# Performance work log

Measured on AMD Instinct MI355X. Metric: run time of the kernel, lower is better.

Reference implementation:

```python
import jax, jax.numpy as jnp
import numpy as np

B, T, C = 8, 2048, 1024  # micro_bsz, seq_len, n_embd (== complexsize)


def setup_inputs() -> dict:
    key = jax.random.key(0)
    ks = jax.random.split(key, 6)
    w = lambda k, shape: (jax.random.normal(k, shape, dtype=jnp.float32) * 0.02)
    return {
        "x": jax.random.normal(ks[0], (B, T, C), dtype=jnp.float32),
        "Wk": w(ks[1], (2 * C, C)),      # key: n_embd -> 2*n_embd (no bias)
        "Wa": w(ks[2], (C, 2 * C)),      # activation: 2*n_embd -> n_embd (no bias)
        "Wf": w(ks[3], (2, C, C)),       # WaveNet filter conv, kernel=2, WIO layout
        "Wg": w(ks[4], (2, C, C)),       # WaveNet gate conv, kernel=2, WIO layout
        "Wo": w(ks[5], (C, C)),          # WaveNet 1x1 output projection
    }


def _causal_conv(x, W):
    # x: [B,T,Cin], W: [K,Cin,Cout]; left-pad K-1 for causality
    return jax.lax.conv_general_dilated(
        x, W, window_strides=(1,), padding=[(W.shape[0] - 1, 0)],
        dimension_numbers=("NWC", "WIO", "NWC"))


def _wavenet_short(x, Wf, Wg, Wo):
    # undialated gated WaveNet unit: tanh(conv_f(x)) * sigmoid(conv_g(x)) -> 1x1 proj
    h = jnp.tanh(_causal_conv(x, Wf)) * jax.nn.sigmoid(_causal_conv(x, Wg))
    return h @ Wo.T


def reference(x, Wk, Wa, Wf, Wg, Wo):
    Bx, Tx, Cx = x.shape
    k = (x @ Wk.T).reshape(Bx, Tx, Cx, 2)                 # [B,T,C,2]
    cv = jax.lax.complex(k[..., 0], k[..., 1])            # view_as_complex -> [B,T,C]
    scale = jax.lax.cummax(jnp.abs(cv), axis=1)           # running max of magnitude
    cv2 = cv / scale.astype(cv.dtype)                      # normalize magnitude <= 1
    kv = jnp.cumprod(cv2, axis=1)                          # complex cumulative product
    re = jnp.stack([kv.real, kv.imag], axis=-1).reshape(Bx, Tx, 2 * Cx)  # view_as_real
    return (re @ Wa.T) * _wavenet_short(x * scale, Wf, Wg, Wo)
```

## Files before the change

### kernel.cpp

```cpp
#include <hip/hip_runtime.h>
#include <cmath>

#define T_SEQ 2048
#define C_DIM 1024

typedef unsigned short u16;
typedef unsigned int u32;
typedef short bf16x8 __attribute__((ext_vector_type(8)));
typedef _Float16 f16x8 __attribute__((ext_vector_type(8)));
typedef float f32x4 __attribute__((ext_vector_type(4)));
typedef unsigned short u16x8 __attribute__((ext_vector_type(8)));

#define AS1 __attribute__((address_space(1)))
#define AS3 __attribute__((address_space(3)))

__device__ __forceinline__ u16 f2bf(float f) {
    u32 u = __builtin_bit_cast(u32, f);
    u32 r = u + 0x7fffu + ((u >> 16) & 1u);
    return (u16)(r >> 16);
}
__device__ __forceinline__ u16 f2h(float f) {
    return __builtin_bit_cast(u16, (_Float16)f);
}
__device__ __forceinline__ float h2f(u16 h) {
    return (float)__builtin_bit_cast(_Float16, h);
}
__device__ __forceinline__ void gl_lds16(const void* g, void* l) {
    __builtin_amdgcn_global_load_lds((const AS1 u32*)g, (AS3 u32*)l, 16, 0, 0);
}

__device__ __forceinline__ int xcd_swz(int lin, int nwg) {
    return (lin & 7) * (nwg >> 3) + (lin >> 3);
}

#define SBAR() do { __builtin_amdgcn_sched_barrier(0); \
                    __builtin_amdgcn_s_barrier(); \
                    __builtin_amdgcn_sched_barrier(0); } while (0)
#define VMC(n) do { asm volatile("s_waitcnt vmcnt(" #n ")" ::: "memory"); \
                    __builtin_amdgcn_sched_barrier(0); } while (0)
#define LGKM0() do { asm volatile("s_waitcnt lgkmcnt(0)" ::: "memory"); \
                     __builtin_amdgcn_sched_barrier(0); } while (0)

template<int DT, int EPI>
__global__ __launch_bounds__(512, 2)
void gemm8(const u16* __restrict__ Ap, const u16* __restrict__ Bp,
           void* __restrict__ Cout, const u16* __restrict__ Cmul,
           int M, int N, int K)
{
    __shared__ u16 lds[2 * 32768];
    const int tid  = threadIdx.x;
    const int lane = tid & 63;
    const int wid  = tid >> 6;
    const int wrow = wid >> 2;
    const int wcol = wid & 3;
    const int gx = gridDim.x;
    const int lin = xcd_swz(blockIdx.x + gx * blockIdx.y, gx * gridDim.y);
    const int m0 = (lin / gx) * 256;
    const int n0 = (lin % gx) * 256;
    const int NT = K / 64;

    f32x4 acc[8][4] = {};

    auto stageu = [&](int t, int u) {
        const int isB = u & 1, kh = u >> 1;
        u16* ubase = &lds[(t & 1) * 32768 + isB * 16384 + kh * 8192];
        const u16* src = isB ? Bp + (size_t)n0 * K : Ap + (size_t)m0 * K;
        const int k0 = t * 64 + kh * 32;
        #pragma unroll
        for (int j = 0; j < 2; ++j) {
            const int c = wid + 8 * j;
            const int p = c * 64 + lane;
            const int row = p >> 2;
            const int sp  = (p & 3) ^ ((row >> 1) & 3);
            gl_lds16(src + (size_t)row * K + k0 + sp * 8, ubase + c * 512);
        }
    };

    auto lda = [&](int buf, int kh, int mq, u16x8 (&a)[4]) {
        const u16* base = &lds[buf * 32768 + kh * 8192];
        #pragma unroll
        for (int f = 0; f < 4; ++f) {
            const int row = wrow * 128 + mq * 64 + f * 16 + (lane & 15);
            const int sp  = (lane >> 4) ^ ((row >> 1) & 3);
            a[f] = *(const u16x8*)&base[row * 32 + sp * 8];
        }
    };
    auto ldb = [&](int buf, int kh, u16x8 (&b)[4]) {
        const u16* base = &lds[buf * 32768 + 16384 + kh * 8192];
        #pragma unroll
        for (int f = 0; f < 4; ++f) {
            const int row = wcol * 64 + f * 16 + (lane & 15);
            const int sp  = (lane >> 4) ^ ((row >> 1) & 3);
            b[f] = *(const u16x8*)&base[row * 32 + sp * 8];
        }
    };
    auto mm = [&](const u16x8 (&a)[4], const u16x8 (&b)[4], int mq) {
        __builtin_amdgcn_s_setprio(1);
        #pragma unroll
        for (int fm = 0; fm < 4; ++fm)
            #pragma unroll
            for (int fn = 0; fn < 4; ++fn) {
                if constexpr (DT == 1)
                    acc[mq * 4 + fm][fn] = __builtin_amdgcn_mfma_f32_16x16x32_f16(
                        __builtin_bit_cast(f16x8, a[fm]), __builtin_bit_cast(f16x8, b[fn]),
                        acc[mq * 4 + fm][fn], 0, 0, 0);
                else
                    acc[mq * 4 + fm][fn] = __builtin_amdgcn_mfma_f32_16x16x32_bf16(
                        __builtin_bit_cast(bf16x8, a[fm]), __builtin_bit_cast(bf16x8, b[fn]),
                        acc[mq * 4 + fm][fn], 0, 0, 0);
            }
        __builtin_amdgcn_s_setprio(0);
    };

    stageu(0, 0); stageu(0, 1); stageu(0, 2); stageu(0, 3);
    VMC(0);
    SBAR();

    u16x8 a[4], b[4];
    for (int t = 0; t < NT; ++t) {
        const int buf = t & 1;
        const bool more = (t + 1 < NT);
        lda(buf, 0, 0, a); ldb(buf, 0, b);
        if (more) stageu(t + 1, 0);
        SBAR(); LGKM0();
        mm(a, b, 0);
        SBAR();
        lda(buf, 0, 1, a);
        if (more) { stageu(t + 1, 1); VMC(4); } else { VMC(0); }
        SBAR(); LGKM0();
        mm(a, b, 1);
        SBAR();
        lda(buf, 1, 0, a); ldb(buf, 1, b);
        if (more) stageu(t + 1, 2);
        SBAR(); LGKM0();
        mm(a, b, 0);
        SBAR();
        lda(buf, 1, 1, a);
        if (more) { stageu(t + 1, 3); VMC(4); }
        SBAR(); LGKM0();
        mm(a, b, 1);
        SBAR();
    }

    const int crow0 = m0 + wrow * 128 + ((lane >> 4) << 2);
    const int ccol  = n0 + wcol * 64 + (lane & 15);
    #pragma unroll
    for (int mi = 0; mi < 8; ++mi)
        #pragma unroll
        for (int fn = 0; fn < 4; ++fn)
            #pragma unroll
            for (int r = 0; r < 4; ++r) {
                const size_t idx = (size_t)(crow0 + mi * 16 + r) * N + ccol + fn * 16;
                if constexpr (EPI == 0)
                    ((u16*)Cout)[idx] = f2h(acc[mi][fn][r]);
                else
                    ((float*)Cout)[idx] = h2f(Cmul[idx]) * acc[mi][fn][r];
            }
}

__global__ __launch_bounds__(512, 2)
void conv8(const u16* __restrict__ A, const u16* __restrict__ Wfgt,
           u16* __restrict__ H, int M)
{
    __shared__ u16 lds[2 * 32768];
    const int tid  = threadIdx.x;
    const int lane = tid & 63;
    const int wid  = tid >> 6;
    const int wrow = wid >> 1;
    const int wcol = wid & 1;
    const int gx = gridDim.x;
    const int lin = xcd_swz(blockIdx.x + gx * blockIdx.y, gx * gridDim.y);
    const int m0 = (lin / gx) * 256;
    const int n0 = (lin % gx) * 128;
    const int NT = 32;

    f32x4 accF[4][4] = {};
    f32x4 accG[4][4] = {};

    auto stageA = [&](int t, int kh) {
        u16* ubase = &lds[(t & 1) * 32768 + kh * 8192];
        const int tap = t >> 4;
        const int k0 = (t & 15) * 64 + kh * 32;
        const int sh = (tap == 0) ? 1 : 0;
        #pragma unroll
        for (int j = 0; j < 2; ++j) {
            const int c = wid + 8 * j;
            const int p = c * 64 + lane;
            const int row = p >> 2;
            const int sp  = (p & 3) ^ ((row >> 1) & 3);
            int grow = m0 + row - sh;
            if (grow < 0) grow = 0;
            gl_lds16(A + (size_t)grow * C_DIM + k0 + sp * 8, ubase + c * 512);
        }
    };
    auto stageB = [&](int t, int kh) {
        u16* ubase = &lds[(t & 1) * 32768 + 16384 + kh * 8192];
        const int tap = t >> 4;
        const int k0 = (t & 15) * 64 + kh * 32;
        const u16* BF = Wfgt + (size_t)tap * 2 * C_DIM * C_DIM;
        const u16* BG = BF + (size_t)C_DIM * C_DIM;
        #pragma unroll
        for (int j = 0; j < 2; ++j) {
            const int c = wid + 8 * j;
            const int isG = c >> 3;
            const int p = (c & 7) * 64 + lane;
            const int row = p >> 2;
            const int sp  = (p & 3) ^ ((row >> 1) & 3);
            const u16* src = (isG ? BG : BF) + (size_t)(n0 + row) * C_DIM + k0 + sp * 8;
            gl_lds16(src, ubase + isG * 4096 + (c & 7) * 512);
        }
    };

    auto lda4 = [&](int buf, int kh, bf16x8 (&a)[4]) {
        const u16* base = &lds[buf * 32768 + kh * 8192];
        #pragma unroll
        for (int f = 0; f < 4; ++f) {
            const int row = wrow * 64 + f * 16 + (lane & 15);
            const int sp  = (lane >> 4) ^ ((row >> 1) & 3);
            a[f] = *(const bf16x8*)&base[row * 32 + sp * 8];
        }
    };
    auto ldb4 = [&](int buf, int kh, int isG, bf16x8 (&b)[4]) {
        const u16* base = &lds[buf * 32768 + 16384 + kh * 8192 + isG * 4096];
        #pragma unroll
        for (int f = 0; f < 4; ++f) {
            const int row = wcol * 64 + f * 16 + (lane & 15);
            const int sp  = (lane >> 4) ^ ((row >> 1) & 3);
            b[f] = *(const bf16x8*)&base[row * 32 + sp * 8];
        }
    };
    auto mm4 = [&](const bf16x8 (&a)[4], const bf16x8 (&b)[4], f32x4 (&acc)[4][4]) {
        #pragma unroll
        for (int fm = 0; fm < 4; ++fm)
            #pragma unroll
            for (int fn = 0; fn < 4; ++fn)
                acc[fm][fn] = __builtin_amdgcn_mfma_f32_16x16x32_bf16(
                    a[fm], b[fn], acc[fm][fn], 0, 0, 0);
    };

    const bool zrow = (m0 % T_SEQ) == 0;
    const bool zlane = (wrow == 0) && ((lane & 15) == 0);
    const bf16x8 zvec = {0,0,0,0,0,0,0,0};

    stageA(0, 0); stageB(0, 0); stageA(0, 1); stageB(0, 1);
    VMC(0);
    SBAR();

    bf16x8 a[4], bF[4], bG[4];
    for (int t = 0; t < NT; ++t) {
        const int buf = t & 1;
        const bool more = (t + 1 < NT);
        const bool z0 = zrow && (t < 16);
        lda4(buf, 0, a); ldb4(buf, 0, 0, bF); ldb4(buf, 0, 1, bG);
        if (more) { stageA(t + 1, 0); stageB(t + 1, 0); VMC(4); } else { VMC(0); }
        SBAR(); LGKM0();
        if (z0 && zlane) a[0] = zvec;
        __builtin_amdgcn_s_setprio(1);
        mm4(a, bF, accF); mm4(a, bG, accG);
        __builtin_amdgcn_s_setprio(0);
        SBAR();
        lda4(buf, 1, a); ldb4(buf, 1, 0, bF); ldb4(buf, 1, 1, bG);
        if (more) { stageA(t + 1, 1); stageB(t + 1, 1); VMC(4); } else { VMC(0); }
        SBAR(); LGKM0();
        if (z0 && zlane) a[0] = zvec;
        __builtin_amdgcn_s_setprio(1);
        mm4(a, bF, accF); mm4(a, bG, accG);
        __builtin_amdgcn_s_setprio(0);
        SBAR();
    }

    const int crow0 = m0 + wrow * 64 + ((lane >> 4) << 2);
    const int ccol  = n0 + wcol * 64 + (lane & 15);
    #pragma unroll
    for (int fm = 0; fm < 4; ++fm)
        #pragma unroll
        for (int fn = 0; fn < 4; ++fn)
            #pragma unroll
            for (int r = 0; r < 4; ++r) {
                const float fv = accF[fm][fn][r];
                const float gv = accG[fm][fn][r];
                const float th = 1.0f - 2.0f / (expf(2.0f * fv) + 1.0f);
                const float sg = 1.0f / (1.0f + expf(-gv));
                H[(size_t)(crow0 + fm * 16 + r) * C_DIM + ccol + fn * 16] = f2bf(th * sg);
            }
}

#define SSEG 32
#define SCHB 32
#define SSL (T_SEQ / SSEG)

__global__ __launch_bounds__(1024, 1)
void scan_kernel(u16* __restrict__ kq, u16* __restrict__ xyb)
{
    __shared__ float  lmax[SSEG][SCHB];
    __shared__ float2 lprod[SSEG][SCHB];
    const int blk = blockIdx.x;
    const int b   = blk >> 5;
    const int c0  = (blk & 31) * SCHB;
    const int ch  = threadIdx.x & (SCHB - 1);
    const int seg = threadIdx.x >> 5;
    const int c   = c0 + ch;
    const int t0  = seg * SSL;
    const size_t baseh = (size_t)b * T_SEQ * 2048 + 2 * c + (size_t)t0 * 2048;
    const size_t base1 = (size_t)b * T_SEQ * C_DIM + c + (size_t)t0 * C_DIM;

    float m2 = 0.f;
    {
        size_t idx = baseh;
        for (int g = 0; g < SSL / 4; ++g) {
            const u32 v0 = *(const u32*)&kq[idx];
            const u32 v1 = *(const u32*)&kq[idx + 2048];
            const u32 v2 = *(const u32*)&kq[idx + 4096];
            const u32 v3 = *(const u32*)&kq[idx + 6144];
            float re, im;
            re = h2f((u16)(v0 & 0xffffu)); im = h2f((u16)(v0 >> 16)); m2 = fmaxf(m2, re*re + im*im);
            re = h2f((u16)(v1 & 0xffffu)); im = h2f((u16)(v1 >> 16)); m2 = fmaxf(m2, re*re + im*im);
            re = h2f((u16)(v2 & 0xffffu)); im = h2f((u16)(v2 >> 16)); m2 = fmaxf(m2, re*re + im*im);
            re = h2f((u16)(v3 & 0xffffu)); im = h2f((u16)(v3 >> 16)); m2 = fmaxf(m2, re*re + im*im);
            idx += 4 * 2048;
        }
    }
    lmax[seg][ch] = sqrtf(m2);
    __syncthreads();
    #pragma unroll
    for (int s = 1; s < SSEG; s <<= 1) {
        const float v = lmax[seg][ch];
        const float u = (seg >= s) ? lmax[seg - s][ch] : 0.f;
        __syncthreads();
        lmax[seg][ch] = fmaxf(v, u);
        __syncthreads();
    }
    const float premax = (seg > 0) ? lmax[seg - 1][ch] : 0.f;

    float pr = 1.f, pi = 0.f;
    float m = premax;
    {
        size_t idx = baseh, idx1 = base1;
        for (int g = 0; g < SSL / 4; ++g) {
            const u32 v0 = *(const u32*)&kq[idx];
            const u32 v1 = *(const u32*)&kq[idx + 2048];
            const u32 v2 = *(const u32*)&kq[idx + 4096];
            const u32 v3 = *(const u32*)&kq[idx + 6144];
            const u16 x0 = xyb[idx1];
            const u16 x1 = xyb[idx1 + C_DIM];
            const u16 x2 = xyb[idx1 + 2 * C_DIM];
            const u16 x3 = xyb[idx1 + 3 * C_DIM];
            u32 vv[4] = {v0, v1, v2, v3};
            u16 xx[4] = {x0, x1, x2, x3};
            #pragma unroll
            for (int q = 0; q < 4; ++q) {
                const float re = h2f((u16)(vv[q] & 0xffffu));
                const float im = h2f((u16)(vv[q] >> 16));
                m = fmaxf(m, sqrtf(re * re + im * im));
                const float inv = 1.f / m;
                const float r0 = re * inv, r1 = im * inv;
                const float nr = pr * r0 - pi * r1;
                const float ni = pr * r1 + pi * r0;
                pr = nr; pi = ni;
                xyb[idx1 + (size_t)q * C_DIM] = f2bf(h2f(xx[q]) * m);
            }
            idx += 4 * 2048; idx1 += 4 * C_DIM;
        }
    }
    lprod[seg][ch] = make_float2(pr, pi);
    __syncthreads();
    #pragma unroll
    for (int s = 1; s < SSEG; s <<= 1) {
        const float2 v = lprod[seg][ch];
        const float2 u = (seg >= s) ? lprod[seg - s][ch] : make_float2(1.f, 0.f);
        __syncthreads();
        lprod[seg][ch] = make_float2(u.x * v.x - u.y * v.y,
                                     u.x * v.y + u.y * v.x);
        __syncthreads();
    }
    float ppr = 1.f, ppi = 0.f;
    if (seg > 0) { const float2 pp = lprod[seg - 1][ch]; ppr = pp.x; ppi = pp.y; }

    pr = 1.f; pi = 0.f;
    m = premax;
    {
        size_t idx = baseh;
        for (int g = 0; g < SSL / 4; ++g) {
            const u32 v0 = *(const u32*)&kq[idx];
            const u32 v1 = *(const u32*)&kq[idx + 2048];
            const u32 v2 = *(const u32*)&kq[idx + 4096];
            const u32 v3 = *(const u32*)&kq[idx + 6144];
            u32 vv[4] = {v0, v1, v2, v3};
            u32 ww[4];
            #pragma unroll
            for (int q = 0; q < 4; ++q) {
                const float re = h2f((u16)(vv[q] & 0xffffu));
                const float im = h2f((u16)(vv[q] >> 16));
                m = fmaxf(m, sqrtf(re * re + im * im));
                const float inv = 1.f / m;
                const float r0 = re * inv, r1 = im * inv;
                const float nr = pr * r0 - pi * r1;
                const float ni = pr * r1 + pi * r0;
                pr = nr; pi = ni;
                const float fr = ppr * nr - ppi * ni;
                const float fi = ppr * ni + ppi * nr;
                ww[q] = ((u32)f2bf(fi) << 16) | (u32)f2bf(fr);
            }
            *(u32*)&kq[idx]        = ww[0];
            *(u32*)&kq[idx + 2048] = ww[1];
            *(u32*)&kq[idx + 4096] = ww[2];
            *(u32*)&kq[idx + 6144] = ww[3];
            idx += 4 * 2048;
        }
    }
}

__global__ void cvt_weights(const float* __restrict__ Wk, const float* __restrict__ Wa,
                            const float* __restrict__ Wo, u16* __restrict__ Wkh,
                            u16* __restrict__ Wab, u16* __restrict__ Wob)
{
    const int n1 = 2048 * 1024, n2 = 2 * 2048 * 1024, n3 = n2 + 1024 * 1024;
    const int i = (blockIdx.x * blockDim.x + threadIdx.x) * 4;
    if (i < n1) {
        const float4 v = *(const float4*)&Wk[i];
        ushort4 o; o.x = f2h(v.x); o.y = f2h(v.y); o.z = f2h(v.z); o.w = f2h(v.w);
        *(ushort4*)&Wkh[i] = o;
    } else if (i < n2) {
        const int j = i - n1;
        const float4 v = *(const float4*)&Wa[j];
        ushort4 o; o.x = f2bf(v.x); o.y = f2bf(v.y); o.z = f2bf(v.z); o.w = f2bf(v.w);
        *(ushort4*)&Wab[j] = o;
    } else if (i < n3) {
        const int j = i - n2;
        const float4 v = *(const float4*)&Wo[j];
        ushort4 o; o.x = f2bf(v.x); o.y = f2bf(v.y); o.z = f2bf(v.z); o.w = f2bf(v.w);
        *(ushort4*)&Wob[j] = o;
    }
}

__global__ void cvt_f16(const float* __restrict__ src, u16* __restrict__ dst, int n)
{
    const int i = (blockIdx.x * blockDim.x + threadIdx.x) * 4;
    if (i >= n) return;
    const float4 v = *(const float4*)&src[i];
    ushort4 o;
    o.x = f2h(v.x); o.y = f2h(v.y); o.z = f2h(v.z); o.w = f2h(v.w);
    *(ushort4*)&dst[i] = o;
}

__global__ __launch_bounds__(256)
void wtrans(const float* __restrict__ Wf, const float* __restrict__ Wg,
            u16* __restrict__ dst)
{
    __shared__ float tile[64][65];
    const int z = blockIdx.z;
    const float* src = ((z < 2) ? Wf : Wg) + (size_t)(z & 1) * C_DIM * C_DIM;
    u16* d = dst + (size_t)(z & 1) * (2 * C_DIM) * C_DIM
                 + ((z < 2) ? (size_t)0 : (size_t)C_DIM * C_DIM);
    const int k0 = blockIdx.x * 64;
    const int n0 = blockIdx.y * 64;
    const int tx = threadIdx.x & 63, ty = threadIdx.x >> 6;
    #pragma unroll
    for (int i = 0; i < 16; ++i) {
        const int r = ty + i * 4;
        tile[r][tx] = src[(size_t)(k0 + r) * C_DIM + n0 + tx];
    }
    __syncthreads();
    #pragma unroll
    for (int i = 0; i < 16; ++i) {
        const int r = ty + i * 4;
        d[(size_t)(n0 + r) * C_DIM + k0 + tx] = f2bf(tile[tx][r]);
    }
}

extern "C" void kernel_launch(void* const* d_in, const int* in_sizes, int n_in,
                              void* d_out, int out_size, void* d_ws, size_t ws_size,
                              hipStream_t stream)
{
    const float* x  = (const float*)d_in[0];
    const float* Wk = (const float*)d_in[1];
    const float* Wa = (const float*)d_in[2];
    const float* Wf = (const float*)d_in[3];
    const float* Wg = (const float*)d_in[4];
    const float* Wo = (const float*)d_in[5];
    float* out = (float*)d_out;

    const int M = 8 * T_SEQ;
    u16* kq   = (u16*)d_ws;
    u16* yb   = (u16*)((char*)d_ws + 67108864ull);
    u16* hb   = (u16*)((char*)d_ws + 100663296ull);
    u16* Wkh  = (u16*)((char*)d_ws + 134217728ull);
    u16* Wab  = Wkh + 2048 * 1024;
    u16* Wfgt = Wab + 2048 * 1024;
    u16* Wob  = Wfgt + 2ull * 2048 * 1024;
    u16* acth = (u16*)((char*)d_ws + 153092096ull);

    cvt_weights<<<(5 * 1024 * 1024 / 4 + 255) / 256, 256, 0, stream>>>(
        Wk, Wa, Wo, Wkh, Wab, Wob);
    wtrans  <<<dim3(16, 16, 4), 256, 0, stream>>>(Wf, Wg, Wfgt);
    cvt_f16 <<<(M * 1024 / 4) / 256, 256, 0, stream>>>(x, yb, M * 1024);

    gemm8<1, 0><<<dim3(2048 / 256, M / 256), 512, 0, stream>>>(
        yb, Wkh, kq, nullptr, M, 2048, 1024);

    scan_kernel<<<256, 1024, 0, stream>>>(kq, yb);

    gemm8<0, 0><<<dim3(1024 / 256, M / 256), 512, 0, stream>>>(
        kq, Wab, acth, nullptr, M, 1024, 2048);

    conv8<<<dim3(1024 / 128, M / 256), 512, 0, stream>>>(yb, Wfgt, hb, M);

    gemm8<0, 1><<<dim3(1024 / 256, M / 256), 512, 0, stream>>>(
        hb, Wob, out, acth, M, 1024, 1024);
}
```

Baseline: 441.7 us.

## Split fused filter/gate conv into two 256x256-tiled conv kernels

The fused conv kernel, which computed filter and gate accumulators together on 256x128 tiles, is replaced by two launches of a templated kernel that each use 256x256 tiles with a 2x4 wave layout and 8x4 accumulator fragments. The first launch writes the filter pre-activation as fp16 into the reused kq workspace. The second computes the gate, reads the filter values back, and applies tanh times sigmoid. The goal is a better MFMA-to-load ratio per tile, at the cost of reading the activations twice and an extra M x 1024 fp16 write and read round trip.

```diff
diff --git a/kernel.cpp b/kernel.cpp
--- a/kernel.cpp
+++ b/kernel.cpp
@@ -158,70 +158,68 @@
             }
 }
 
+template<int GATE>
 __global__ __launch_bounds__(512, 2)
-void conv8(const u16* __restrict__ A, const u16* __restrict__ Wfgt,
-           u16* __restrict__ H, int M)
-{
+void conv_g8(const u16* __restrict__ Ap, const u16* __restrict__ Wfgt,
+             u16* __restrict__ Hout, const u16* __restrict__ Fh, int M)
+{
+    constexpr int N = 1024;
     __shared__ u16 lds[2 * 32768];
     const int tid  = threadIdx.x;
     const int lane = tid & 63;
     const int wid  = tid >> 6;
-    const int wrow = wid >> 1;
-    const int wcol = wid & 1;
+    const int wrow = wid >> 2;
+    const int wcol = wid & 3;
     const int gx = gridDim.x;
     const int lin = xcd_swz(blockIdx.x + gx * blockIdx.y, gx * gridDim.y);
     const int m0 = (lin / gx) * 256;
-    const int n0 = (lin % gx) * 128;
+    const int n0 = (lin % gx) * 256;
     const int NT = 32;
 
-    f32x4 accF[4][4] = {};
-    f32x4 accG[4][4] = {};
-
-    auto stageA = [&](int t, int kh) {
-        u16* ubase = &lds[(t & 1) * 32768 + kh * 8192];
+    f32x4 acc[8][4] = {};
+
+    auto stageu = [&](int t, int u) {
+        const int isB = u & 1, kh = u >> 1;
+        u16* ubase = &lds[(t & 1) * 32768 + isB * 16384 + kh * 8192];
         const int tap = t >> 4;
         const int k0 = (t & 15) * 64 + kh * 32;
-        const int sh = (tap == 0) ? 1 : 0;
-        #pragma unroll
-        for (int j = 0; j < 2; ++j) {
-            const int c = wid + 8 * j;
-            const int p = c * 64 + lane;
-            const int row = p >> 2;
-            const int sp  = (p & 3) ^ ((row >> 1) & 3);
-            int grow = m0 + row - sh;
-            if (grow < 0) grow = 0;
-            gl_lds16(A + (size_t)grow * C_DIM + k0 + sp * 8, ubase + c * 512);
-        }
-    };
-    auto stageB = [&](int t, int kh) {
-        u16* ubase = &lds[(t & 1) * 32768 + 16384 + kh * 8192];
-        const int tap = t >> 4;
-        const int k0 = (t & 15) * 64 + kh * 32;
-        const u16* BF = Wfgt + (size_t)tap * 2 * C_DIM * C_DIM;
-        const u16* BG = BF + (size_t)C_DIM * C_DIM;
-        #pragma unroll
-        for (int j = 0; j < 2; ++j) {
-            const int c = wid + 8 * j;
-            const int isG = c >> 3;
-            const int p = (c & 7) * 64 + lane;
-            const int row = p >> 2;
-            const int sp  = (p & 3) ^ ((row >> 1) & 3);
-            const u16* src = (isG ? BG : BF) + (size_t)(n0 + row) * C_DIM + k0 + sp * 8;
-            gl_lds16(src, ubase + isG * 4096 + (c & 7) * 512);
-        }
-    };
-
-    auto lda4 = [&](int buf, int kh, bf16x8 (&a)[4]) {
+        if (isB) {
+            const u16* src = Wfgt + (size_t)tap * 2 * C_DIM * C_DIM
+                           + (size_t)GATE * C_DIM * C_DIM + (size_t)n0 * C_DIM;
+            #pragma unroll
+            for (int j = 0; j < 2; ++j) {
+                const int c = wid + 8 * j;
+                const int p = c * 64 + lane;
+                const int row = p >> 2;
+                const int sp  = (p & 3) ^ ((row >> 1) & 3);
+                gl_lds16(src + (size_t)row * C_DIM + k0 + sp * 8, ubase + c * 512);
+            }
+        } else {
+            const int sh = (tap == 0) ? 1 : 0;
+            #pragma unroll
+            for (int j = 0; j < 2; ++j) {
+                const int c = wid + 8 * j;
+                const int p = c * 64 + lane;
+                const int row = p >> 2;
+                const int sp  = (p & 3) ^ ((row >> 1) & 3);
+                int grow = m0 + row - sh;
+                if (grow < 0) grow = 0;
+                gl_lds16(Ap + (size_t)grow * C_DIM + k0 + sp * 8, ubase + c * 512);
+            }
+        }
+    };
+
+    auto lda = [&](int buf, int kh, int mq, bf16x8 (&a)[4]) {
         const u16* base = &lds[buf * 32768 + kh * 8192];
         #pragma unroll
         for (int f = 0; f < 4; ++f) {
-            const int row = wrow * 64 + f * 16 + (lane & 15);
+            const int row = wrow * 128 + mq * 64 + f * 16 + (lane & 15);
             const int sp  = (lane >> 4) ^ ((row >> 1) & 3);
             a[f] = *(const bf16x8*)&base[row * 32 + sp * 8];
         }
     };
-    auto ldb4 = [&](int buf, int kh, int isG, bf16x8 (&b)[4]) {
-        const u16* base = &lds[buf * 32768 + 16384 + kh * 8192 + isG * 4096];
+    auto ldb = [&](int buf, int kh, bf16x8 (&b)[4]) {
+        const u16* base = &lds[buf * 32768 + 16384 + kh * 8192];
         #pragma unroll
         for (int f = 0; f < 4; ++f) {
             const int row = wcol * 64 + f * 16 + (lane & 15);
@@ -229,59 +227,72 @@
             b[f] = *(const bf16x8*)&base[row * 32 + sp * 8];
         }
     };
-    auto mm4 = [&](const bf16x8 (&a)[4], const bf16x8 (&b)[4], f32x4 (&acc)[4][4]) {
+    auto mm = [&](const bf16x8 (&a)[4], const bf16x8 (&b)[4], int mq) {
+        __builtin_amdgcn_s_setprio(1);
         #pragma unroll
         for (int fm = 0; fm < 4; ++fm)
             #pragma unroll
             for (int fn = 0; fn < 4; ++fn)
-                acc[fm][fn] = __builtin_amdgcn_mfma_f32_16x16x32_bf16(
-                    a[fm], b[fn], acc[fm][fn], 0, 0, 0);
-    };
-
-    const bool zrow = (m0 % T_SEQ) == 0;
+                acc[mq * 4 + fm][fn] = __builtin_amdgcn_mfma_f32_16x16x32_bf16(
+                    a[fm], b[fn], acc[mq * 4 + fm][fn], 0, 0, 0);
+        __builtin_amdgcn_s_setprio(0);
+    };
+
+    const bool zrow  = (m0 % T_SEQ) == 0;
     const bool zlane = (wrow == 0) && ((lane & 15) == 0);
     const bf16x8 zvec = {0,0,0,0,0,0,0,0};
 
-    stageA(0, 0); stageB(0, 0); stageA(0, 1); stageB(0, 1);
+    stageu(0, 0); stageu(0, 1); stageu(0, 2); stageu(0, 3);
     VMC(0);
     SBAR();
 
-    bf16x8 a[4], bF[4], bG[4];
+    bf16x8 a[4], b[4];
     for (int t = 0; t < NT; ++t) {
         const int buf = t & 1;
         const bool more = (t + 1 < NT);
         const bool z0 = zrow && (t < 16);
-        lda4(buf, 0, a); ldb4(buf, 0, 0, bF); ldb4(buf, 0, 1, bG);
-        if (more) { stageA(t + 1, 0); stageB(t + 1, 0); VMC(4); } else { VMC(0); }
+        lda(buf, 0, 0, a); ldb(buf, 0, b);
+        if (more) stageu(t + 1, 0);
         SBAR(); LGKM0();
         if (z0 && zlane) a[0] = zvec;
-        __builtin_amdgcn_s_setprio(1);
-        mm4(a, bF, accF); mm4(a, bG, accG);
-        __builtin_amdgcn_s_setprio(0);
-        SBAR();
-        lda4(buf, 1, a); ldb4(buf, 1, 0, bF); ldb4(buf, 1, 1, bG);
-        if (more) { stageA(t + 1, 1); stageB(t + 1, 1); VMC(4); } else { VMC(0); }
+        mm(a, b, 0);
+        SBAR();
+        lda(buf, 0, 1, a);
+        if (more) { stageu(t + 1, 1); VMC(4); } else { VMC(0); }
+        SBAR(); LGKM0();
+        mm(a, b, 1);
+        SBAR();
+        lda(buf, 1, 0, a); ldb(buf, 1, b);
+        if (more) stageu(t + 1, 2);
         SBAR(); LGKM0();
         if (z0 && zlane) a[0] = zvec;
-        __builtin_amdgcn_s_setprio(1);
-        mm4(a, bF, accF); mm4(a, bG, accG);
-        __builtin_amdgcn_s_setprio(0);
-        SBAR();
-    }
-
-    const int crow0 = m0 + wrow * 64 + ((lane >> 4) << 2);
+        mm(a, b, 0);
+        SBAR();
+        lda(buf, 1, 1, a);
+        if (more) { stageu(t + 1, 3); VMC(4); }
+        SBAR(); LGKM0();
+        mm(a, b, 1);
+        SBAR();
+    }
+
+    const int crow0 = m0 + wrow * 128 + ((lane >> 4) << 2);
     const int ccol  = n0 + wcol * 64 + (lane & 15);
     #pragma unroll
-    for (int fm = 0; fm < 4; ++fm)
+    for (int mi = 0; mi < 8; ++mi)
         #pragma unroll
         for (int fn = 0; fn < 4; ++fn)
             #pragma unroll
             for (int r = 0; r < 4; ++r) {
-                const float fv = accF[fm][fn][r];
-                const float gv = accG[fm][fn][r];
-                const float th = 1.0f - 2.0f / (expf(2.0f * fv) + 1.0f);
-                const float sg = 1.0f / (1.0f + expf(-gv));
-                H[(size_t)(crow0 + fm * 16 + r) * C_DIM + ccol + fn * 16] = f2bf(th * sg);
+                const size_t idx = (size_t)(crow0 + mi * 16 + r) * N + ccol + fn * 16;
+                if constexpr (GATE == 0) {
+                    Hout[idx] = f2h(acc[mi][fn][r]);
+                } else {
+                    const float fv = h2f(Fh[idx]);
+                    const float gv = acc[mi][fn][r];
+                    const float th = 1.0f - 2.0f / (expf(2.0f * fv) + 1.0f);
+                    const float sg = 1.0f / (1.0f + expf(-gv));
+                    Hout[idx] = f2bf(th * sg);
+                }
             }
 }
 
@@ -482,6 +493,7 @@
 
     const int M = 8 * T_SEQ;
     u16* kq   = (u16*)d_ws;
+    u16* Fh   = (u16*)d_ws;
     u16* yb   = (u16*)((char*)d_ws + 67108864ull);
     u16* hb   = (u16*)((char*)d_ws + 100663296ull);
     u16* Wkh  = (u16*)((char*)d_ws + 134217728ull);
@@ -503,7 +515,11 @@
     gemm8<0, 0><<<dim3(1024 / 256, M / 256), 512, 0, stream>>>(
         kq, Wab, acth, nullptr, M, 1024, 2048);
 
-    conv8<<<dim3(1024 / 128, M / 256), 512, 0, stream>>>(yb, Wfgt, hb, M);
+    conv_g8<0><<<dim3(1024 / 256, M / 256), 512, 0, stream>>>(
+        yb, Wfgt, Fh, nullptr, M);
+
+    conv_g8<1><<<dim3(1024 / 256, M / 256), 512, 0, stream>>>(
+        yb, Wfgt, hb, Fh, M);
 
     gemm8<0, 1><<<dim3(1024 / 256, M / 256), 512, 0, stream>>>(
         hb, Wob, out, acth, M, 1024, 1024);
```

Result: slower. 452.8 us (+2.5%).
